# Performance work log

Measured on AMD Instinct MI355X. Metric: run time of the kernel, lower is better.

Reference implementation:

```python
import jax, jax.numpy as jnp
import numpy as np

N = 100000  # number of nodes
E = 3200000  # number of edges (avg degree 32)


def spmm(rows, cols, vals, Y):
    # sparse A (COO) @ dense Y : gather rows of Y at cols, scale, scatter-add to rows
    return jax.ops.segment_sum(vals[:, None] * Y[cols], rows, num_segments=N)


def setup_inputs() -> dict:
    key = jax.random.key(0)
    kx, kr, kc, kv, k0, k1 = jax.random.split(key, 6)
    X = jax.random.normal(kx, (N, 512), dtype=jnp.float32)
    edge_rows = jax.random.randint(kr, (E,), 0, N, dtype=jnp.int32)
    edge_cols = jax.random.randint(kc, (E,), 0, N, dtype=jnp.int32)
    edge_vals = jax.random.uniform(kv, (E,), dtype=jnp.float32)
    W0 = jax.random.normal(k0, (512, 256), dtype=jnp.float32) * 0.05
    W1 = jax.random.normal(k1, (256, 64), dtype=jnp.float32) * 0.05
    return {"X": X, "edge_rows": edge_rows, "edge_cols": edge_cols,
            "edge_vals": edge_vals, "W0": W0, "W1": W1}


def reference(X, edge_rows, edge_cols, edge_vals, W0, W1):
    # layer 1: A_hat @ (X W0), relu
    H1 = jax.nn.relu(spmm(edge_rows, edge_cols, edge_vals, X @ W0))  # [N, H]
    # layer 2: A_hat @ (H1 W1), softmax over classes
    Z = spmm(edge_rows, edge_cols, edge_vals, H1 @ W1)  # [N, F]
    return jax.nn.softmax(Z, axis=-1)
```

## Files before the change

### kernel.cpp

```cpp
#include <hip/hip_runtime.h>
#include <hip/hip_bf16.h>
#include <hip/hip_fp16.h>
#include <cstdint>

#define N_NODES 100000
#define N_EDGES 3200000
#define F_IN    512
#define F_HID   256
#define F_OUT   64
#define CAP     96

#define G_SCATTER 12500
#define G_GEMM1   3125
#define LDS_STRIDE 272

typedef _Float16 half8_t __attribute__((ext_vector_type(8)));
typedef _Float16 half4_t __attribute__((ext_vector_type(4)));
typedef float    float4_t __attribute__((ext_vector_type(4)));


__global__ __launch_bounds__(256) void prep_kernel(
    const float* __restrict__ W0, const float* __restrict__ W1,
    _Float16* __restrict__ W0T, _Float16* __restrict__ W1T,
    int* __restrict__ cursor) {
    int i = blockIdx.x * 256 + threadIdx.x;
    if (i < N_NODES) cursor[i] = 0;
    if (i < F_HID * F_IN) {
        int n = i >> 9, k = i & 511;
        W0T[i] = (_Float16)W0[k * F_HID + n];
    }
    int j = i - F_HID * F_IN;
    if (j >= 0 && j < F_OUT * F_HID) {
        int n = j >> 8, k = j & 255;
        W1T[j] = (_Float16)W1[k * F_OUT + n];
    }
}


__global__ __launch_bounds__(256, 6) void mega_kernel(
    const int* __restrict__ erows, const int* __restrict__ ecols,
    const float* __restrict__ evals, int* __restrict__ cursor,
    int2* __restrict__ ell,
    const float* __restrict__ X, const _Float16* __restrict__ W0T,
    _Float16* __restrict__ H0) {

    if (blockIdx.x < G_SCATTER) {
        int e = blockIdx.x * 256 + threadIdx.x;
        int r = erows[e];
        int p = atomicAdd(&cursor[r], 1);
        if (p < CAP)
            ell[(size_t)r * CAP + p] = make_int2(ecols[e], __float_as_int(evals[e]));
        return;
    }

    const int blk  = blockIdx.x - G_SCATTER;
    const int wave = threadIdx.x >> 6;
    const int lane = threadIdx.x & 63;
    const int l15  = lane & 15;
    const int quad = lane >> 4;
    const int m0   = blk * 32;
    const int n0   = wave * 64;

    float4_t acc[2][4] = {};

    for (int k0 = 0; k0 < F_IN; k0 += 32) {
        const int kk = k0 + quad * 8;
        half8_t b[4];
        #pragma unroll
        for (int nt = 0; nt < 4; nt++)
            b[nt] = *(const half8_t*)(W0T + (size_t)(n0 + nt * 16 + l15) * F_IN + kk);

        half8_t a[2];
        #pragma unroll
        for (int mt = 0; mt < 2; mt++) {
            const float* p = X + (size_t)(m0 + mt * 16 + l15) * F_IN + kk;
            float4_t lo = *(const float4_t*)p;
            float4_t hi = *(const float4_t*)(p + 4);
            half8_t f;
            f[0] = (_Float16)lo[0]; f[1] = (_Float16)lo[1];
            f[2] = (_Float16)lo[2]; f[3] = (_Float16)lo[3];
            f[4] = (_Float16)hi[0]; f[5] = (_Float16)hi[1];
            f[6] = (_Float16)hi[2]; f[7] = (_Float16)hi[3];
            a[mt] = f;
        }

        #pragma unroll
        for (int mt = 0; mt < 2; mt++)
            #pragma unroll
            for (int nt = 0; nt < 4; nt++)
                acc[mt][nt] = __builtin_amdgcn_mfma_f32_16x16x32_f16(
                    a[mt], b[nt], acc[mt][nt], 0, 0, 0);
    }

    #pragma unroll
    for (int mt = 0; mt < 2; mt++)
        #pragma unroll
        for (int reg = 0; reg < 4; reg++) {
            int m = m0 + mt * 16 + quad * 4 + reg;
            #pragma unroll
            for (int nt = 0; nt < 4; nt++)
                H0[(size_t)m * F_HID + n0 + nt * 16 + l15] =
                    (_Float16)acc[mt][nt][reg];
        }
}


__global__ __launch_bounds__(256) void spmm_relu_gemm2_kernel(
    const _Float16* __restrict__ H0, const int2* __restrict__ ell,
    const int* __restrict__ cursor, const _Float16* __restrict__ W1T,
    _Float16* __restrict__ H2) {
    __shared__ _Float16 hrow[16][LDS_STRIDE];

    const int wave = threadIdx.x >> 6;
    const int t    = threadIdx.x & 63;
    const int base = blockIdx.x * 16;
    const half4_t* H0v = (const half4_t*)H0;

    for (int rr = 0; rr < 4; rr++) {
        const int local = wave * 4 + rr;
        const int r = base + local;
        int n = cursor[r]; if (n > CAP) n = CAP;
        const int2* cv = ell + (size_t)r * CAP;

        float4_t acc = {};
        int j = 0;
        for (; j + 4 <= n; j += 4) {
            int4 e0 = *(const int4*)(cv + j);
            int4 e1 = *(const int4*)(cv + j + 2);
            half4_t g0 = H0v[(size_t)e0.x * 64 + t];
            half4_t g1 = H0v[(size_t)e0.z * 64 + t];
            half4_t g2 = H0v[(size_t)e1.x * 64 + t];
            half4_t g3 = H0v[(size_t)e1.z * 64 + t];
            float v0 = __int_as_float(e0.y), v1 = __int_as_float(e0.w);
            float v2 = __int_as_float(e1.y), v3 = __int_as_float(e1.w);
            #pragma unroll
            for (int i = 0; i < 4; i++) {
                acc[i] = fmaf(v0, (float)g0[i], acc[i]);
                acc[i] = fmaf(v1, (float)g1[i], acc[i]);
                acc[i] = fmaf(v2, (float)g2[i], acc[i]);
                acc[i] = fmaf(v3, (float)g3[i], acc[i]);
            }
        }
        for (; j < n; j++) {
            int2 e = cv[j];
            half4_t g = H0v[(size_t)e.x * 64 + t];
            float vv = __int_as_float(e.y);
            #pragma unroll
            for (int i = 0; i < 4; i++) acc[i] = fmaf(vv, (float)g[i], acc[i]);
        }
        half4_t o;
        #pragma unroll
        for (int i = 0; i < 4; i++) o[i] = (_Float16)fmaxf(acc[i], 0.f);
        *(half4_t*)(&hrow[local][t * 4]) = o;
    }
    __syncthreads();

    const int l15  = t & 15;
    const int quad = t >> 4;
    float4_t acc2 = {};
    #pragma unroll
    for (int k0 = 0; k0 < F_HID; k0 += 32) {
        const int kk = k0 + quad * 8;
        half8_t a = *(const half8_t*)(&hrow[l15][kk]);
        half8_t b = *(const half8_t*)(W1T + (size_t)(wave * 16 + l15) * F_HID + kk);
        acc2 = __builtin_amdgcn_mfma_f32_16x16x32_f16(a, b, acc2, 0, 0, 0);
    }
    #pragma unroll
    for (int reg = 0; reg < 4; reg++) {
        int m = base + quad * 4 + reg;
        H2[(size_t)m * F_OUT + wave * 16 + l15] = (_Float16)acc2[reg];
    }
}


__global__ __launch_bounds__(256) void spmm_softmax_kernel(
    const _Float16* __restrict__ H2, const int2* __restrict__ ell,
    const int* __restrict__ cursor, float* __restrict__ out) {
    const int lane = threadIdx.x & 63;
    const int r = blockIdx.x * 4 + (threadIdx.x >> 6);
    int n = cursor[r]; if (n > CAP) n = CAP;
    const int2* cv = ell + (size_t)r * CAP;

    float acc = 0.f;
    int j = 0;
    for (; j + 4 <= n; j += 4) {
        int4 e0 = *(const int4*)(cv + j);
        int4 e1 = *(const int4*)(cv + j + 2);
        acc = fmaf(__int_as_float(e0.y), (float)H2[(size_t)e0.x * F_OUT + lane], acc);
        acc = fmaf(__int_as_float(e0.w), (float)H2[(size_t)e0.z * F_OUT + lane], acc);
        acc = fmaf(__int_as_float(e1.y), (float)H2[(size_t)e1.x * F_OUT + lane], acc);
        acc = fmaf(__int_as_float(e1.w), (float)H2[(size_t)e1.z * F_OUT + lane], acc);
    }
    for (; j < n; j++) {
        int2 e = cv[j];
        acc = fmaf(__int_as_float(e.y), (float)H2[(size_t)e.x * F_OUT + lane], acc);
    }

    float m = acc;
    #pragma unroll
    for (int o = 32; o >= 1; o >>= 1) m = fmaxf(m, __shfl_xor(m, o, 64));
    float e = expf(acc - m);
    float s = e;
    #pragma unroll
    for (int o = 32; o >= 1; o >>= 1) s += __shfl_xor(s, o, 64);
    out[(size_t)r * F_OUT + lane] = e / s;
}


extern "C" void kernel_launch(void* const* d_in, const int* in_sizes, int n_in,
                              void* d_out, int out_size, void* d_ws, size_t ws_size,
                              hipStream_t stream) {
    const float* X     = (const float*)d_in[0];
    const int*   erows = (const int*)  d_in[1];
    const int*   ecols = (const int*)  d_in[2];
    const float* evals = (const float*)d_in[3];
    const float* W0    = (const float*)d_in[4];
    const float* W1    = (const float*)d_in[5];
    float* out = (float*)d_out;

    char* p = (char*)d_ws;
    _Float16* H0  = (_Float16*)p; p += (size_t)N_NODES * F_HID * 2;
    _Float16* H2  = (_Float16*)p; p += (size_t)N_NODES * F_OUT * 2;
    _Float16* W0T = (_Float16*)p; p += (size_t)F_HID * F_IN * 2;
    _Float16* W1T = (_Float16*)p; p += (size_t)F_OUT * F_HID * 2;
    int*  cursor  = (int*)p;      p += (size_t)N_NODES * 4;
    int2* ell     = (int2*)p;

    prep_kernel<<<576, 256, 0, stream>>>(W0, W1, W0T, W1T, cursor);

    mega_kernel<<<G_SCATTER + G_GEMM1, 256, 0, stream>>>(
        erows, ecols, evals, cursor, ell, X, W0T, H0);

    spmm_relu_gemm2_kernel<<<N_NODES / 16, 256, 0, stream>>>(H0, ell, cursor, W1T, H2);

    spmm_softmax_kernel<<<N_NODES / 4, 256, 0, stream>>>(H2, ell, cursor, out);
}
```

Measured before the change: 1.007 ms.

## Split mega kernel, shard ELL scatter, enlarge GEMM1 tiles, slice H0 layout for gathers

Splits the fused scatter+GEMM kernel into separate launches. The ELL scatter now runs four row-shard passes over all edges, each pass touching only a quarter of the rows, so atomics and writes stay localized. GEMM1 uses 64-row tiles with clamped boundary rows. H0 is stored as four feature slabs of 64 columns each, and the SpMM gathers slab by slab with 16 threads per row, so each pass touches a smaller working set that may fit better in cache. The cost is reading the edge list four times and losing the overlap between scatter and GEMM.

```diff
diff --git a/kernel.cpp b/kernel.cpp
--- a/kernel.cpp
+++ b/kernel.cpp
@@ -10,8 +10,10 @@
 #define F_OUT   64
 #define CAP     96
 
+#define NSHARD   4
+#define SHARD_SZ 25000
 #define G_SCATTER 12500
-#define G_GEMM1   3125
+#define NSLICE   4
 #define LDS_STRIDE 272
 
 typedef _Float16 half8_t __attribute__((ext_vector_type(8)));
@@ -37,31 +39,38 @@
 }
 
 
-__global__ __launch_bounds__(256, 6) void mega_kernel(
+__global__ __launch_bounds__(256) void ell_scatter_kernel(
     const int* __restrict__ erows, const int* __restrict__ ecols,
     const float* __restrict__ evals, int* __restrict__ cursor,
-    int2* __restrict__ ell,
+    int2* __restrict__ ell) {
+    const int shard = blockIdx.x / G_SCATTER;
+    const int e = (blockIdx.x % G_SCATTER) * 256 + threadIdx.x;
+    int r = erows[e];
+    if (r / SHARD_SZ != shard) return;
+    int p = atomicAdd(&cursor[r], 1);
+    if (p < CAP)
+        ell[(size_t)r * CAP + p] = make_int2(ecols[e], __float_as_int(evals[e]));
+}
+
+
+__global__ __launch_bounds__(256) void gemm1_mfma_kernel(
     const float* __restrict__ X, const _Float16* __restrict__ W0T,
     _Float16* __restrict__ H0) {
-
-    if (blockIdx.x < G_SCATTER) {
-        int e = blockIdx.x * 256 + threadIdx.x;
-        int r = erows[e];
-        int p = atomicAdd(&cursor[r], 1);
-        if (p < CAP)
-            ell[(size_t)r * CAP + p] = make_int2(ecols[e], __float_as_int(evals[e]));
-        return;
-    }
-
-    const int blk  = blockIdx.x - G_SCATTER;
     const int wave = threadIdx.x >> 6;
     const int lane = threadIdx.x & 63;
     const int l15  = lane & 15;
     const int quad = lane >> 4;
-    const int m0   = blk * 32;
+    const int m0   = blockIdx.x * 64;
     const int n0   = wave * 64;
 
-    float4_t acc[2][4] = {};
+    float4_t acc[4][4] = {};
+
+    int row[4];
+    #pragma unroll
+    for (int mt = 0; mt < 4; mt++) {
+        int r = m0 + mt * 16 + l15;
+        row[mt] = r < N_NODES ? r : N_NODES - 1;
+    }
 
     for (int k0 = 0; k0 < F_IN; k0 += 32) {
         const int kk = k0 + quad * 8;
@@ -70,10 +79,10 @@
         for (int nt = 0; nt < 4; nt++)
             b[nt] = *(const half8_t*)(W0T + (size_t)(n0 + nt * 16 + l15) * F_IN + kk);
 
-        half8_t a[2];
-        #pragma unroll
-        for (int mt = 0; mt < 2; mt++) {
-            const float* p = X + (size_t)(m0 + mt * 16 + l15) * F_IN + kk;
+        half8_t a[4];
+        #pragma unroll
+        for (int mt = 0; mt < 4; mt++) {
+            const float* p = X + (size_t)row[mt] * F_IN + kk;
             float4_t lo = *(const float4_t*)p;
             float4_t hi = *(const float4_t*)(p + 4);
             half8_t f;
@@ -85,7 +94,7 @@
         }
 
         #pragma unroll
-        for (int mt = 0; mt < 2; mt++)
+        for (int mt = 0; mt < 4; mt++)
             #pragma unroll
             for (int nt = 0; nt < 4; nt++)
                 acc[mt][nt] = __builtin_amdgcn_mfma_f32_16x16x32_f16(
@@ -93,14 +102,16 @@
     }
 
     #pragma unroll
-    for (int mt = 0; mt < 2; mt++)
+    for (int mt = 0; mt < 4; mt++)
         #pragma unroll
         for (int reg = 0; reg < 4; reg++) {
             int m = m0 + mt * 16 + quad * 4 + reg;
-            #pragma unroll
-            for (int nt = 0; nt < 4; nt++)
-                H0[(size_t)m * F_HID + n0 + nt * 16 + l15] =
-                    (_Float16)acc[mt][nt][reg];
+            if (m < N_NODES) {
+                #pragma unroll
+                for (int nt = 0; nt < 4; nt++)
+                    H0[((size_t)wave * N_NODES + m) * 64 + nt * 16 + l15] =
+                        (_Float16)acc[mt][nt][reg];
+            }
         }
 }
 
@@ -111,26 +122,26 @@
     _Float16* __restrict__ H2) {
     __shared__ _Float16 hrow[16][LDS_STRIDE];
 
-    const int wave = threadIdx.x >> 6;
     const int t    = threadIdx.x & 63;
+    const int grp  = threadIdx.x >> 4;
+    const int sub  = threadIdx.x & 15;
     const int base = blockIdx.x * 16;
-    const half4_t* H0v = (const half4_t*)H0;
-
-    for (int rr = 0; rr < 4; rr++) {
-        const int local = wave * 4 + rr;
-        const int r = base + local;
-        int n = cursor[r]; if (n > CAP) n = CAP;
-        const int2* cv = ell + (size_t)r * CAP;
-
+    const int r    = base + grp;
+
+    int n = cursor[r]; if (n > CAP) n = CAP;
+    const int2* cv = ell + (size_t)r * CAP;
+
+    for (int s = 0; s < NSLICE; s++) {
+        const half4_t* slab = (const half4_t*)(H0 + (size_t)s * N_NODES * 64);
         float4_t acc = {};
         int j = 0;
         for (; j + 4 <= n; j += 4) {
             int4 e0 = *(const int4*)(cv + j);
             int4 e1 = *(const int4*)(cv + j + 2);
-            half4_t g0 = H0v[(size_t)e0.x * 64 + t];
-            half4_t g1 = H0v[(size_t)e0.z * 64 + t];
-            half4_t g2 = H0v[(size_t)e1.x * 64 + t];
-            half4_t g3 = H0v[(size_t)e1.z * 64 + t];
+            half4_t g0 = slab[(size_t)e0.x * 16 + sub];
+            half4_t g1 = slab[(size_t)e0.z * 16 + sub];
+            half4_t g2 = slab[(size_t)e1.x * 16 + sub];
+            half4_t g3 = slab[(size_t)e1.z * 16 + sub];
             float v0 = __int_as_float(e0.y), v1 = __int_as_float(e0.w);
             float v2 = __int_as_float(e1.y), v3 = __int_as_float(e1.w);
             #pragma unroll
@@ -143,7 +154,7 @@
         }
         for (; j < n; j++) {
             int2 e = cv[j];
-            half4_t g = H0v[(size_t)e.x * 64 + t];
+            half4_t g = slab[(size_t)e.x * 16 + sub];
             float vv = __int_as_float(e.y);
             #pragma unroll
             for (int i = 0; i < 4; i++) acc[i] = fmaf(vv, (float)g[i], acc[i]);
@@ -151,10 +162,11 @@
         half4_t o;
         #pragma unroll
         for (int i = 0; i < 4; i++) o[i] = (_Float16)fmaxf(acc[i], 0.f);
-        *(half4_t*)(&hrow[local][t * 4]) = o;
+        *(half4_t*)(&hrow[grp][s * 64 + sub * 4]) = o;
     }
     __syncthreads();
 
+    const int wave = threadIdx.x >> 6;
     const int l15  = t & 15;
     const int quad = t >> 4;
     float4_t acc2 = {};
@@ -228,8 +240,10 @@
 
     prep_kernel<<<576, 256, 0, stream>>>(W0, W1, W0T, W1T, cursor);
 
-    mega_kernel<<<G_SCATTER + G_GEMM1, 256, 0, stream>>>(
-        erows, ecols, evals, cursor, ell, X, W0T, H0);
+    ell_scatter_kernel<<<NSHARD * G_SCATTER, 256, 0, stream>>>(
+        erows, ecols, evals, cursor, ell);
+
+    gemm1_mfma_kernel<<<(N_NODES + 63) / 64, 256, 0, stream>>>(X, W0T, H0);
 
     spmm_relu_gemm2_kernel<<<N_NODES / 16, 256, 0, stream>>>(H0, ell, cursor, W1T, H2);
 
```

Measured after the change: 934.6 us. 7.2% less time.
